# Performance work log

Measured on AMD Instinct MI355X. Metric: run time of the kernel, lower is better.

## Reference

```python
import jax, jax.numpy as jnp
import numpy as np

N = 100000
E = 1600000
DIMS = [128, 128, 64]


def _gcn_norm(edge_index, num_nodes):
    # PyG gcn_norm: add self-loops, symmetric normalization D^-1/2 (A+I) D^-1/2
    src, dst = edge_index[0], edge_index[1]
    loop = jnp.arange(num_nodes, dtype=src.dtype)
    src = jnp.concatenate([src, loop])
    dst = jnp.concatenate([dst, loop])
    deg = jax.ops.segment_sum(jnp.ones_like(src, dtype=jnp.float32), dst,
                              num_segments=num_nodes)
    dinv = jnp.where(deg > 0, jax.lax.rsqrt(deg), 0.0)
    w = dinv[src] * dinv[dst]  # [E+N]
    return src, dst, w


def _gcn_conv(x, src, dst, w, W, b):
    # transform first (cheaper when out_dim <= in_dim), then aggregate
    h = x @ W                                   # [N, out]
    msg = h[src] * w[:, None]                   # gather + scale  [E+N, out]
    out = jax.ops.segment_sum(msg, dst, num_segments=x.shape[0])
    return out + b


def setup_inputs() -> dict:
    key = jax.random.key(0)
    ks = jax.random.split(key, 6)
    x = jax.random.normal(ks[0], (N, DIMS[0]), dtype=jnp.float32)
    edge_index = jax.random.randint(ks[1], (2, E), 0, N, dtype=jnp.int64)
    # Glorot-style init for GCNConv weights, zero bias (PyG default)
    W1 = jax.random.normal(ks[2], (DIMS[0], DIMS[1]), dtype=jnp.float32) / np.sqrt(DIMS[0])
    b1 = jnp.zeros((DIMS[1],), dtype=jnp.float32)
    W2 = jax.random.normal(ks[3], (DIMS[1], DIMS[2]), dtype=jnp.float32) / np.sqrt(DIMS[1])
    b2 = jnp.zeros((DIMS[2],), dtype=jnp.float32)
    return {"x": x, "edge_index": edge_index, "W1": W1, "b1": b1, "W2": W2, "b2": b2}


def reference(x, edge_index, W1, b1, W2, b2):
    src, dst, w = _gcn_norm(edge_index, x.shape[0])
    h = _gcn_conv(x, src, dst, w, W1, b1)
    h = jax.nn.relu(h)
    # dropout is identity in eval mode (deterministic reference)
    out = _gcn_conv(h, src, dst, w, W2, b2)
    return out
```

## Files before the change

kernel.cpp:

```cpp
#include <hip/hip_runtime.h>
#include <hip/hip_fp16.h>

#define TPB 256
#define CHUNK 1024
#define EPB 4096
#define CSHIFT 8

typedef _Float16 half8 __attribute__((ext_vector_type(8)));
typedef float    f32x4 __attribute__((ext_vector_type(4)));


__global__ __launch_bounds__(256) void scanA_kernel(const int* __restrict__ cnt,
                                                    int* __restrict__ row_ptr,
                                                    int* __restrict__ chunk_sums, int n) {
    __shared__ int ls[256];
    const int t    = threadIdx.x;
    const int base = blockIdx.x * CHUNK;
    const int idx  = base + t * 4;
    int4 v = make_int4(0, 0, 0, 0);
    if (idx + 3 < n) v = *(const int4*)(cnt + idx);
    else {
        if (idx + 0 < n) v.x = cnt[idx + 0];
        if (idx + 1 < n) v.y = cnt[idx + 1];
        if (idx + 2 < n) v.z = cnt[idx + 2];
        if (idx + 3 < n) v.w = cnt[idx + 3];
    }
    int s0 = v.x, s1 = s0 + v.y, s2 = s1 + v.z, s3 = s2 + v.w;
    ls[t] = s3;
    __syncthreads();
    for (int off = 1; off < 256; off <<= 1) {
        int xv = (t >= off) ? ls[t - off] : 0;
        __syncthreads();
        ls[t] += xv;
        __syncthreads();
    }
    int excl = (t == 0) ? 0 : ls[t - 1];
    if (idx + 0 < n) row_ptr[idx + 0] = excl;
    if (idx + 1 < n) row_ptr[idx + 1] = excl + s0;
    if (idx + 2 < n) row_ptr[idx + 2] = excl + s1;
    if (idx + 3 < n) row_ptr[idx + 3] = excl + s2;
    if (t == 255) chunk_sums[blockIdx.x] = ls[255];
}

__global__ __launch_bounds__(256) void scanB_kernel(int* __restrict__ chunk_sums, int nch) {
    __shared__ int ls[256];
    const int t = threadIdx.x;
    ls[t] = (t < nch) ? chunk_sums[t] : 0;
    __syncthreads();
    for (int off = 1; off < 256; off <<= 1) {
        int xv = (t >= off) ? ls[t - off] : 0;
        __syncthreads();
        ls[t] += xv;
        __syncthreads();
    }
    if (t < nch) chunk_sums[t] = (t == 0) ? 0 : ls[t - 1];
}

__global__ __launch_bounds__(256) void scanC_kernel(int* __restrict__ row_ptr,
                                                    const int* __restrict__ chunk_sums, int n) {
    const int base = blockIdx.x * CHUNK;
    const int off  = chunk_sums[blockIdx.x];
    for (int k = threadIdx.x; k < CHUNK; k += 256) {
        int i = base + k;
        if (i < n) row_ptr[i] += off;
    }
}


__global__ __launch_bounds__(256) void hist_kernel(const int* __restrict__ dst,
                                                   int* __restrict__ hist_g,
                                                   int e, int nbc, int nblk) {
    __shared__ int hs[512];
    const int t = threadIdx.x;
    for (int i = t; i < nbc; i += 256) hs[i] = 0;
    __syncthreads();
    const int e0  = blockIdx.x * EPB;
    const int lim = min(e0 + EPB, e);
    for (int i = e0 + t; i < lim; i += 256)
        atomicAdd(&hs[dst[i] >> CSHIFT], 1);
    __syncthreads();
    for (int b = t; b < nbc; b += 256)
        hist_g[b * nblk + blockIdx.x] = hs[b];
}

__global__ __launch_bounds__(256) void partition_kernel(const int* __restrict__ src,
                                                        const int* __restrict__ dst,
                                                        const int* __restrict__ hist_scan,
                                                        int* __restrict__ pairs,
                                                        int e, int nbc, int nblk) {
    __shared__ int  hs[512];
    __shared__ int  lscan[512];
    __shared__ int  lfill[512];
    __shared__ int  base_s[512];
    __shared__ int  ls[256];
    __shared__ int2 sp[EPB];
    const int t = threadIdx.x;
    for (int i = t; i < nbc; i += 256) { hs[i] = 0; lfill[i] = 0; }
    __syncthreads();
    const int e0  = blockIdx.x * EPB;
    const int lim = min(e0 + EPB, e);
    for (int i = e0 + t; i < lim; i += 256)
        atomicAdd(&hs[dst[i] >> CSHIFT], 1);
    __syncthreads();
    int v0 = (2 * t     < nbc) ? hs[2 * t]     : 0;
    int v1 = (2 * t + 1 < nbc) ? hs[2 * t + 1] : 0;
    ls[t] = v0 + v1;
    __syncthreads();
    for (int off = 1; off < 256; off <<= 1) {
        int xv = (t >= off) ? ls[t - off] : 0;
        __syncthreads();
        ls[t] += xv;
        __syncthreads();
    }
    int excl = (t == 0) ? 0 : ls[t - 1];
    if (2 * t     < nbc) lscan[2 * t]     = excl;
    if (2 * t + 1 < nbc) lscan[2 * t + 1] = excl + v0;
    for (int b = t; b < nbc; b += 256) base_s[b] = hist_scan[b * nblk + blockIdx.x];
    __syncthreads();
    for (int i = e0 + t; i < lim; i += 256) {
        int d = dst[i];
        int b = d >> CSHIFT;
        int r = atomicAdd(&lfill[b], 1);
        sp[lscan[b] + r] = make_int2(src[i], d);
    }
    __syncthreads();
    const int cnt = lim - e0;
    for (int i = t; i < cnt; i += 256) {
        int2 pr = sp[i];
        int  b  = pr.y >> CSHIFT;
        pairs[base_s[b] + (i - lscan[b])] = pr.x | ((pr.y & 255) << 17);
    }
}

__global__ __launch_bounds__(256) void bucket_finalize_kernel(const int* __restrict__ pairs,
                                                              const int* __restrict__ hist_scan,
                                                              int* __restrict__ row_ptr,
                                                              float* __restrict__ dinv,
                                                              int* __restrict__ csr_src,
                                                              int n, int e, int nbc, int nblk) {
    __shared__ int cnt_s[256];
    __shared__ int fill[256];
    __shared__ int ls[256];
    const int b   = blockIdx.x;
    const int nb0 = b << CSHIFT;
    const int t   = threadIdx.x;
    const int r0  = hist_scan[b * nblk];
    const int r1  = (b + 1 < nbc) ? hist_scan[(b + 1) * nblk] : e;
    cnt_s[t] = 0;
    __syncthreads();
    for (int i = r0 + t; i < r1; i += 256)
        atomicAdd(&cnt_s[pairs[i] >> 17], 1);
    __syncthreads();
    int c = cnt_s[t];
    ls[t] = c;
    __syncthreads();
    for (int off = 1; off < 256; off <<= 1) {
        int xv = (t >= off) ? ls[t - off] : 0;
        __syncthreads();
        ls[t] += xv;
        __syncthreads();
    }
    int excl = (t == 0) ? 0 : ls[t - 1];
    int node = nb0 + t;
    if (node < n) {
        row_ptr[node] = r0 + excl;
        dinv[node]    = rsqrtf((float)(c + 1));
    }
    fill[t] = r0 + excl;
    __syncthreads();
    for (int i = r0 + t; i < r1; i += 256) {
        int pr = pairs[i];
        int p  = atomicAdd(&fill[pr >> 17], 1);
        csr_src[p] = pr & 0x1FFFF;
    }
    if (b == 0 && t == 0) row_ptr[n] = e;
}


template <int M, bool RELU>
__global__ __launch_bounds__(256) void gemm_mfma_kernel(const float* __restrict__ X,
                                                        const float* __restrict__ W,
                                                        const float* __restrict__ dinv,
                                                        __half* __restrict__ H, int nrows) {
    constexpr int NC = M / 16;
    __shared__ __align__(16) _Float16 Wf[NC * 4 * 64 * 8];

    const int tid = threadIdx.x;

    for (int f = tid; f < NC * 4 * 64; f += 256) {
        int c    = f >> 8;
        int i    = (f >> 6) & 3;
        int lane = f & 63;
        int quad = lane >> 4, n = lane & 15;
        const float* wp = W + (size_t)(i * 32 + quad * 8) * M + c * 16 + n;
        half8 hv;
#pragma unroll
        for (int j = 0; j < 8; ++j) hv[j] = (_Float16)wp[(size_t)j * M];
        ((half8*)Wf)[f] = hv;
    }
    __syncthreads();

    const int  wave = tid >> 6, lane = tid & 63;
    const int  quad = lane >> 4, n16 = lane & 15;
    const long rowbase = (long)blockIdx.x * 64 + wave * 16;

    long arow = rowbase + n16;
    const float4* xr = (const float4*)(X + (arow < nrows ? arow : 0) * 128);
    half8 a[4];
#pragma unroll
    for (int i = 0; i < 4; ++i) {
        float4 x0 = xr[i * 8 + quad * 2];
        float4 x1 = xr[i * 8 + quad * 2 + 1];
        if (RELU) {
            x0.x = fmaxf(x0.x, 0.f); x0.y = fmaxf(x0.y, 0.f);
            x0.z = fmaxf(x0.z, 0.f); x0.w = fmaxf(x0.w, 0.f);
            x1.x = fmaxf(x1.x, 0.f); x1.y = fmaxf(x1.y, 0.f);
            x1.z = fmaxf(x1.z, 0.f); x1.w = fmaxf(x1.w, 0.f);
        }
        half8 hv;
        hv[0] = (_Float16)x0.x; hv[1] = (_Float16)x0.y;
        hv[2] = (_Float16)x0.z; hv[3] = (_Float16)x0.w;
        hv[4] = (_Float16)x1.x; hv[5] = (_Float16)x1.y;
        hv[6] = (_Float16)x1.z; hv[7] = (_Float16)x1.w;
        a[i] = hv;
    }

    float dv[4];
#pragma unroll
    for (int r = 0; r < 4; ++r) {
        long orow = rowbase + quad * 4 + r;
        dv[r] = (orow < nrows) ? dinv[orow] : 0.f;
    }

    for (int c = 0; c < NC; ++c) {
        f32x4 acc = {0.f, 0.f, 0.f, 0.f};
#pragma unroll
        for (int i = 0; i < 4; ++i) {
            half8 b = ((const half8*)Wf)[(c * 4 + i) * 64 + lane];
            acc = __builtin_amdgcn_mfma_f32_16x16x32_f16(a[i], b, acc, 0, 0, 0);
        }
#pragma unroll
        for (int r = 0; r < 4; ++r) {
            long orow = rowbase + quad * 4 + r;
            if (orow < nrows)
                H[orow * M + c * 16 + n16] = __float2half(acc[r] * dv[r]);
        }
    }
}


template <int M>
__global__ __launch_bounds__(TPB) void agg_pull_kernel(const __half* __restrict__ hs,
                                                       const int* __restrict__ csr_src,
                                                       const int* __restrict__ row_ptr,
                                                       const float* __restrict__ dinv,
                                                       const float* __restrict__ bias,
                                                       float* __restrict__ out, int n) {
    const int node = blockIdx.x * (TPB / 64) + (threadIdx.x >> 6);
    const int lane = threadIdx.x & 63;
    if (node >= n) return;
    const int beg = row_ptr[node];
    const int end = row_ptr[node + 1];

    if constexpr (M == 128) {
        const __half2* hp = (const __half2*)hs;
        float2 a[16];
#pragma unroll
        for (int r = 1; r < 16; ++r) a[r] = make_float2(0.f, 0.f);
        a[0] = __half22float2(hp[(long)node * 64 + lane]);
        for (int base = beg; base < end; base += 64) {
            int m = end - base; if (m > 64) m = 64;
            int idx = (lane < m) ? csr_src[base + lane] : 0;
            int j = 0;
            for (; j + 16 <= m; j += 16) {
#pragma unroll
                for (int r = 0; r < 16; ++r) {
                    int s = __shfl(idx, j + r);
                    float2 v = __half22float2(hp[(long)s * 64 + lane]);
                    a[r].x += v.x; a[r].y += v.y;
                }
            }
            for (; j + 4 <= m; j += 4) {
#pragma unroll
                for (int r = 0; r < 4; ++r) {
                    int s = __shfl(idx, j + r);
                    float2 v = __half22float2(hp[(long)s * 64 + lane]);
                    a[r].x += v.x; a[r].y += v.y;
                }
            }
            for (; j < m; ++j) {
                int s = __shfl(idx, j);
                float2 v = __half22float2(hp[(long)s * 64 + lane]);
                a[0].x += v.x; a[0].y += v.y;
            }
        }
#pragma unroll
        for (int r = 8; r < 16; ++r) { a[r - 8].x += a[r].x; a[r - 8].y += a[r].y; }
#pragma unroll
        for (int r = 4; r < 8; ++r) { a[r - 4].x += a[r].x; a[r - 4].y += a[r].y; }
        float  di = dinv[node];
        float2 bv = ((const float2*)bias)[lane];
        float2 o;
        o.x = bv.x + di * ((a[0].x + a[1].x) + (a[2].x + a[3].x));
        o.y = bv.y + di * ((a[0].y + a[1].y) + (a[2].y + a[3].y));
        ((float2*)out)[(long)node * 64 + lane] = o;
    } else {
        float a[16];
#pragma unroll
        for (int r = 1; r < 16; ++r) a[r] = 0.f;
        a[0] = __half2float(hs[(long)node * 64 + lane]);
        for (int base = beg; base < end; base += 64) {
            int m = end - base; if (m > 64) m = 64;
            int idx = (lane < m) ? csr_src[base + lane] : 0;
            int j = 0;
            for (; j + 16 <= m; j += 16) {
#pragma unroll
                for (int r = 0; r < 16; ++r) {
                    int s = __shfl(idx, j + r);
                    a[r] += __half2float(hs[(long)s * 64 + lane]);
                }
            }
            for (; j + 4 <= m; j += 4) {
#pragma unroll
                for (int r = 0; r < 4; ++r) {
                    int s = __shfl(idx, j + r);
                    a[r] += __half2float(hs[(long)s * 64 + lane]);
                }
            }
            for (; j < m; ++j) {
                int s = __shfl(idx, j);
                a[0] += __half2float(hs[(long)s * 64 + lane]);
            }
        }
#pragma unroll
        for (int r = 8; r < 16; ++r) a[r - 8] += a[r];
#pragma unroll
        for (int r = 4; r < 8; ++r) a[r - 4] += a[r];
        float di = dinv[node];
        out[(long)node * 64 + lane] =
            bias[lane] + di * ((a[0] + a[1]) + (a[2] + a[3]));
    }
}


extern "C" void kernel_launch(void* const* d_in, const int* in_sizes, int n_in,
                              void* d_out, int out_size, void* d_ws, size_t ws_size,
                              hipStream_t stream) {
    const float* x  = (const float*)d_in[0];
    const int*   ei = (const int*)d_in[1];
    const float* W1 = (const float*)d_in[2];
    const float* b1 = (const float*)d_in[3];
    const float* W2 = (const float*)d_in[4];
    const float* b2 = (const float*)d_in[5];
    float* out = (float*)d_out;

    const int N = in_sizes[0] / 128;
    const int E = in_sizes[1] / 2;
    const int* srcv = ei;
    const int* dstv = ei + E;

    const int NBC    = (N + 255) >> CSHIFT;
    const int NBLK_E = (E + EPB - 1) / EPB;
    const int HLEN   = NBC * NBLK_E;
    const int NCHH   = (HLEN + CHUNK - 1) / CHUNK;

    char* p = (char*)d_ws;
    int*    row_ptr    = (int*)p;           p += ((size_t)N + 64) * 4;
    int*    chunk_sums = (int*)p;           p += 1024;
    int*    hist       = (int*)p;           p += ((size_t)HLEN + 64) * 4;
    int*    csr_src    = (int*)p;           p += (size_t)E * 4;
    float*  dinv       = (float*)p;         p += ((size_t)N + 64) * 4;
    __half* hs1        = (__half*)p;        p += (size_t)N * 128 * 2;
    float*  out1       = (float*)p;         p += (size_t)N * 128 * 4;
    int*    pairs      = (int*)out1;
    __half* hs2        = hs1;

    hist_kernel<<<NBLK_E, 256, 0, stream>>>(dstv, hist, E, NBC, NBLK_E);
    scanA_kernel<<<NCHH, 256, 0, stream>>>(hist, hist, chunk_sums, HLEN);
    scanB_kernel<<<1, 256, 0, stream>>>(chunk_sums, NCHH);
    scanC_kernel<<<NCHH, 256, 0, stream>>>(hist, chunk_sums, HLEN);
    partition_kernel<<<NBLK_E, 256, 0, stream>>>(srcv, dstv, hist, pairs, E, NBC, NBLK_E);
    bucket_finalize_kernel<<<NBC, 256, 0, stream>>>(pairs, hist, row_ptr, dinv, csr_src,
                                                    N, E, NBC, NBLK_E);

    gemm_mfma_kernel<128, false><<<(N + 63) / 64, 256, 0, stream>>>(x, W1, dinv, hs1, N);
    agg_pull_kernel<128><<<(N + 3) / 4, TPB, 0, stream>>>(hs1, csr_src, row_ptr, dinv, b1, out1, N);

    gemm_mfma_kernel<64, true><<<(N + 63) / 64, 256, 0, stream>>>(out1, W2, dinv, hs2, N);
    agg_pull_kernel<64><<<(N + 3) / 4, TPB, 0, stream>>>(hs2, csr_src, row_ptr, dinv, b2, out, N);
}
```

Baseline: 312.3 us.

## Store layer-1 output in fp16 and use half-wave gathers for 64-wide aggregation

```diff
diff --git a/kernel.cpp b/kernel.cpp
--- a/kernel.cpp
+++ b/kernel.cpp
@@ -177,8 +177,8 @@
 }
 
 
-template <int M, bool RELU>
-__global__ __launch_bounds__(256) void gemm_mfma_kernel(const float* __restrict__ X,
+template <int M, bool RELU, typename XT>
+__global__ __launch_bounds__(256) void gemm_mfma_kernel(const XT* __restrict__ X,
                                                         const float* __restrict__ W,
                                                         const float* __restrict__ dinv,
                                                         __half* __restrict__ H, int nrows) {
@@ -205,24 +205,39 @@
     const long rowbase = (long)blockIdx.x * 64 + wave * 16;
 
     long arow = rowbase + n16;
-    const float4* xr = (const float4*)(X + (arow < nrows ? arow : 0) * 128);
+    const XT* xrow = X + (size_t)(arow < nrows ? arow : 0) * 128;
     half8 a[4];
-#pragma unroll
-    for (int i = 0; i < 4; ++i) {
-        float4 x0 = xr[i * 8 + quad * 2];
-        float4 x1 = xr[i * 8 + quad * 2 + 1];
-        if (RELU) {
-            x0.x = fmaxf(x0.x, 0.f); x0.y = fmaxf(x0.y, 0.f);
-            x0.z = fmaxf(x0.z, 0.f); x0.w = fmaxf(x0.w, 0.f);
-            x1.x = fmaxf(x1.x, 0.f); x1.y = fmaxf(x1.y, 0.f);
-            x1.z = fmaxf(x1.z, 0.f); x1.w = fmaxf(x1.w, 0.f);
-        }
-        half8 hv;
-        hv[0] = (_Float16)x0.x; hv[1] = (_Float16)x0.y;
-        hv[2] = (_Float16)x0.z; hv[3] = (_Float16)x0.w;
-        hv[4] = (_Float16)x1.x; hv[5] = (_Float16)x1.y;
-        hv[6] = (_Float16)x1.z; hv[7] = (_Float16)x1.w;
-        a[i] = hv;
+    if constexpr (sizeof(XT) == 4) {
+        const float4* xr = (const float4*)xrow;
+#pragma unroll
+        for (int i = 0; i < 4; ++i) {
+            float4 x0 = xr[i * 8 + quad * 2];
+            float4 x1 = xr[i * 8 + quad * 2 + 1];
+            if (RELU) {
+                x0.x = fmaxf(x0.x, 0.f); x0.y = fmaxf(x0.y, 0.f);
+                x0.z = fmaxf(x0.z, 0.f); x0.w = fmaxf(x0.w, 0.f);
+                x1.x = fmaxf(x1.x, 0.f); x1.y = fmaxf(x1.y, 0.f);
+                x1.z = fmaxf(x1.z, 0.f); x1.w = fmaxf(x1.w, 0.f);
+            }
+            half8 hv;
+            hv[0] = (_Float16)x0.x; hv[1] = (_Float16)x0.y;
+            hv[2] = (_Float16)x0.z; hv[3] = (_Float16)x0.w;
+            hv[4] = (_Float16)x1.x; hv[5] = (_Float16)x1.y;
+            hv[6] = (_Float16)x1.z; hv[7] = (_Float16)x1.w;
+            a[i] = hv;
+        }
+    } else {
+        const half8* xr = (const half8*)xrow;
+#pragma unroll
+        for (int i = 0; i < 4; ++i) {
+            half8 hv = xr[i * 4 + quad];
+            if (RELU) {
+#pragma unroll
+                for (int j = 0; j < 8; ++j)
+                    hv[j] = (hv[j] > (_Float16)0) ? hv[j] : (_Float16)0;
+            }
+            a[i] = hv;
+        }
     }
 
     float dv[4];
@@ -249,96 +264,118 @@
 }
 
 
-template <int M>
-__global__ __launch_bounds__(TPB) void agg_pull_kernel(const __half* __restrict__ hs,
-                                                       const int* __restrict__ csr_src,
-                                                       const int* __restrict__ row_ptr,
-                                                       const float* __restrict__ dinv,
-                                                       const float* __restrict__ bias,
-                                                       float* __restrict__ out, int n) {
+__global__ __launch_bounds__(TPB) void agg_pull128_kernel(const __half* __restrict__ hs,
+                                                          const int* __restrict__ csr_src,
+                                                          const int* __restrict__ row_ptr,
+                                                          const float* __restrict__ dinv,
+                                                          const float* __restrict__ bias,
+                                                          __half* __restrict__ out, int n) {
     const int node = blockIdx.x * (TPB / 64) + (threadIdx.x >> 6);
     const int lane = threadIdx.x & 63;
     if (node >= n) return;
     const int beg = row_ptr[node];
     const int end = row_ptr[node + 1];
 
-    if constexpr (M == 128) {
-        const __half2* hp = (const __half2*)hs;
-        float2 a[16];
-#pragma unroll
-        for (int r = 1; r < 16; ++r) a[r] = make_float2(0.f, 0.f);
-        a[0] = __half22float2(hp[(long)node * 64 + lane]);
-        for (int base = beg; base < end; base += 64) {
-            int m = end - base; if (m > 64) m = 64;
-            int idx = (lane < m) ? csr_src[base + lane] : 0;
-            int j = 0;
-            for (; j + 16 <= m; j += 16) {
-#pragma unroll
-                for (int r = 0; r < 16; ++r) {
-                    int s = __shfl(idx, j + r);
-                    float2 v = __half22float2(hp[(long)s * 64 + lane]);
-                    a[r].x += v.x; a[r].y += v.y;
-                }
+    const __half2* hp = (const __half2*)hs;
+    float2 a[16];
+#pragma unroll
+    for (int r = 1; r < 16; ++r) a[r] = make_float2(0.f, 0.f);
+    a[0] = __half22float2(hp[(long)node * 64 + lane]);
+    for (int base = beg; base < end; base += 64) {
+        int m = end - base; if (m > 64) m = 64;
+        int idx = (lane < m) ? csr_src[base + lane] : 0;
+        int j = 0;
+        for (; j + 16 <= m; j += 16) {
+#pragma unroll
+            for (int r = 0; r < 16; ++r) {
+                int s = __shfl(idx, j + r);
+                float2 v = __half22float2(hp[(long)s * 64 + lane]);
+                a[r].x += v.x; a[r].y += v.y;
             }
-            for (; j + 4 <= m; j += 4) {
-#pragma unroll
-                for (int r = 0; r < 4; ++r) {
-                    int s = __shfl(idx, j + r);
-                    float2 v = __half22float2(hp[(long)s * 64 + lane]);
-                    a[r].x += v.x; a[r].y += v.y;
-                }
+        }
+        for (; j + 4 <= m; j += 4) {
+#pragma unroll
+            for (int r = 0; r < 4; ++r) {
+                int s = __shfl(idx, j + r);
+                float2 v = __half22float2(hp[(long)s * 64 + lane]);
+                a[r].x += v.x; a[r].y += v.y;
             }
-            for (; j < m; ++j) {
-                int s = __shfl(idx, j);
-                float2 v = __half22float2(hp[(long)s * 64 + lane]);
-                a[0].x += v.x; a[0].y += v.y;
+        }
+        for (; j < m; ++j) {
+            int s = __shfl(idx, j);
+            float2 v = __half22float2(hp[(long)s * 64 + lane]);
+            a[0].x += v.x; a[0].y += v.y;
+        }
+    }
+#pragma unroll
+    for (int r = 8; r < 16; ++r) { a[r - 8].x += a[r].x; a[r - 8].y += a[r].y; }
+#pragma unroll
+    for (int r = 4; r < 8; ++r) { a[r - 4].x += a[r].x; a[r - 4].y += a[r].y; }
+    float  di = dinv[node];
+    float2 bv = ((const float2*)bias)[lane];
+    float ox = bv.x + di * ((a[0].x + a[1].x) + (a[2].x + a[3].x));
+    float oy = bv.y + di * ((a[0].y + a[1].y) + (a[2].y + a[3].y));
+    ((__half2*)out)[(long)node * 64 + lane] = __floats2half2_rn(ox, oy);
+}
+
+
+__global__ __launch_bounds__(TPB) void agg_pull64_kernel(const __half* __restrict__ hs,
+                                                         const int* __restrict__ csr_src,
+                                                         const int* __restrict__ row_ptr,
+                                                         const float* __restrict__ dinv,
+                                                         const float* __restrict__ bias,
+                                                         float* __restrict__ out, int n) {
+    const int node = blockIdx.x * (TPB / 64) + (threadIdx.x >> 6);
+    const int lane = threadIdx.x & 63;
+    if (node >= n) return;
+    const int half = lane >> 5;
+    const int sl   = lane & 31;
+    const int beg = row_ptr[node];
+    const int end = row_ptr[node + 1];
+    const __half2* hp = (const __half2*)hs;
+
+    float2 a[8];
+#pragma unroll
+    for (int r = 0; r < 8; ++r) a[r] = make_float2(0.f, 0.f);
+
+    for (int base = beg; base < end; base += 64) {
+        int m = end - base; if (m > 64) m = 64;
+        int idx = (lane < m) ? csr_src[base + lane] : 0;
+        int j = 0;
+        for (; j + 16 <= m; j += 16) {
+#pragma unroll
+            for (int r = 0; r < 8; ++r) {
+                int s = __shfl(idx, j + 2 * r + half);
+                float2 v = __half22float2(hp[(long)s * 32 + sl]);
+                a[r].x += v.x; a[r].y += v.y;
             }
         }
-#pragma unroll
-        for (int r = 8; r < 16; ++r) { a[r - 8].x += a[r].x; a[r - 8].y += a[r].y; }
-#pragma unroll
-        for (int r = 4; r < 8; ++r) { a[r - 4].x += a[r].x; a[r - 4].y += a[r].y; }
+        for (; j + 2 <= m; j += 2) {
+            int s = __shfl(idx, j + half);
+            float2 v = __half22float2(hp[(long)s * 32 + sl]);
+            a[0].x += v.x; a[0].y += v.y;
+        }
+        if (j < m) {
+            int s = __shfl(idx, j);
+            float2 v = __half22float2(hp[(long)s * 32 + sl]);
+            if (half == 0) { a[0].x += v.x; a[0].y += v.y; }
+        }
+    }
+#pragma unroll
+    for (int r = 4; r < 8; ++r) { a[r - 4].x += a[r].x; a[r - 4].y += a[r].y; }
+    float2 acc;
+    acc.x = (a[0].x + a[1].x) + (a[2].x + a[3].x);
+    acc.y = (a[0].y + a[1].y) + (a[2].y + a[3].y);
+    acc.x += __shfl(acc.x, lane ^ 32);
+    acc.y += __shfl(acc.y, lane ^ 32);
+    if (half == 0) {
+        float2 sv = __half22float2(hp[(long)node * 32 + sl]);
         float  di = dinv[node];
-        float2 bv = ((const float2*)bias)[lane];
+        float2 bv = ((const float2*)bias)[sl];
         float2 o;
-        o.x = bv.x + di * ((a[0].x + a[1].x) + (a[2].x + a[3].x));
-        o.y = bv.y + di * ((a[0].y + a[1].y) + (a[2].y + a[3].y));
-        ((float2*)out)[(long)node * 64 + lane] = o;
-    } else {
-        float a[16];
-#pragma unroll
-        for (int r = 1; r < 16; ++r) a[r] = 0.f;
-        a[0] = __half2float(hs[(long)node * 64 + lane]);
-        for (int base = beg; base < end; base += 64) {
-            int m = end - base; if (m > 64) m = 64;
-            int idx = (lane < m) ? csr_src[base + lane] : 0;
-            int j = 0;
-            for (; j + 16 <= m; j += 16) {
-#pragma unroll
-                for (int r = 0; r < 16; ++r) {
-                    int s = __shfl(idx, j + r);
-                    a[r] += __half2float(hs[(long)s * 64 + lane]);
-                }
-            }
-            for (; j + 4 <= m; j += 4) {
-#pragma unroll
-                for (int r = 0; r < 4; ++r) {
-                    int s = __shfl(idx, j + r);
-                    a[r] += __half2float(hs[(long)s * 64 + lane]);
-                }
-            }
-            for (; j < m; ++j) {
-                int s = __shfl(idx, j);
-                a[0] += __half2float(hs[(long)s * 64 + lane]);
-            }
-        }
-#pragma unroll
-        for (int r = 8; r < 16; ++r) a[r - 8] += a[r];
-#pragma unroll
-        for (int r = 4; r < 8; ++r) a[r - 4] += a[r];
-        float di = dinv[node];
-        out[(long)node * 64 + lane] =
-            bias[lane] + di * ((a[0] + a[1]) + (a[2] + a[3]));
+        o.x = bv.x + di * (acc.x + sv.x);
+        o.y = bv.y + di * (acc.y + sv.y);
+        ((float2*)out)[(long)node * 32 + sl] = o;
     }
 }
 
@@ -371,7 +408,7 @@
     int*    csr_src    = (int*)p;           p += (size_t)E * 4;
     float*  dinv       = (float*)p;         p += ((size_t)N + 64) * 4;
     __half* hs1        = (__half*)p;        p += (size_t)N * 128 * 2;
-    float*  out1       = (float*)p;         p += (size_t)N * 128 * 4;
+    __half* out1       = (__half*)p;        p += (size_t)N * 128 * 2;
     int*    pairs      = (int*)out1;
     __half* hs2        = hs1;
 
@@ -383,9 +420,10 @@
     bucket_finalize_kernel<<<NBC, 256, 0, stream>>>(pairs, hist, row_ptr, dinv, csr_src,
                                                     N, E, NBC, NBLK_E);
 
-    gemm_mfma_kernel<128, false><<<(N + 63) / 64, 256, 0, stream>>>(x, W1, dinv, hs1, N);
-    agg_pull_kernel<128><<<(N + 3) / 4, TPB, 0, stream>>>(hs1, csr_src, row_ptr, dinv, b1, out1, N);
-
-    gemm_mfma_kernel<64, true><<<(N + 63) / 64, 256, 0, stream>>>(out1, W2, dinv, hs2, N);
-    agg_pull_kernel<64><<<(N + 3) / 4, TPB, 0, stream>>>(hs2, csr_src, row_ptr, dinv, b2, out, N);
-}
+    gemm_mfma_kernel<128, false, float><<<(N + 63) / 64, 256, 0, stream>>>(x, W1, dinv, hs1, N);
+    agg_pull128_kernel<<<(N + 3) / 4, TPB, 0, stream>>>(hs1, csr_src, row_ptr, dinv, b1, out1, N);
+
+    gemm_mfma_kernel<64, true, _Float16><<<(N + 63) / 64, 256, 0, stream>>>(
+        (const _Float16*)out1, W2, dinv, hs2, N);
+    agg_pull64_kernel<<<(N + 3) / 4, TPB, 0, stream>>>(hs2, csr_src, row_ptr, dinv, b2, out, N);
+}
```

Result: no change. 308.3 us (-1.3%).
